# Kernel tuning notes

Measured on AMD Instinct MI355X. Metric: run time of the kernel, lower is better.

## Reference

```python
import jax, jax.numpy as jnp
import numpy as np

SEQ, EMBED, H, QLR, KVLR, RD, VD = 4096, 2048, 16, 512, 512, 64, 128
KD = VD + RD  # full key/query head dim (content + rope)


def _make_rotary_pe(seq_len, dim):
    inv_freq = 1.0 / jnp.power(10000.0, jnp.arange(0, dim, 2) / dim)
    t = jnp.arange(seq_len)
    freqs = jnp.outer(t, inv_freq)  # (seq, dim//2)
    return jnp.sin(freqs), jnp.cos(freqs)


def _apply_rope(x, sin, cos):
    # x: (seq, ..., dim); sin/cos: (seq, dim//2)
    d = x.shape[-1] // 2
    x1, x2 = x[..., :d], x[..., d:]
    sin2 = jnp.concatenate([sin, sin], axis=-1)
    cos2 = jnp.concatenate([cos, cos], axis=-1)
    ne = x.ndim - 2
    sin2 = sin2.reshape(sin2.shape[0], *[1] * ne, sin2.shape[1])
    cos2 = cos2.reshape(cos2.shape[0], *[1] * ne, cos2.shape[1])
    rot = jnp.concatenate([-x2, x1], axis=-1)
    return x * cos2 + rot * sin2


def setup_inputs() -> dict:
    key = jax.random.key(0)
    ks = jax.random.split(key, 8)

    def w(k, out_dim, in_dim):
        return jax.random.normal(k, (out_dim, in_dim), dtype=jnp.float32) * (1.0 / np.sqrt(in_dim))

    x = jax.random.normal(ks[0], (SEQ, EMBED), dtype=jnp.float32)
    mask = jnp.tril(jnp.ones((SEQ, SEQ), dtype=bool))  # causal
    return {
        "x": x,
        "mask": mask,
        "w_q_down": w(ks[1], QLR, EMBED),
        "w_q_up": w(ks[2], H * VD, QLR),
        "w_q_rope": w(ks[3], H * RD, QLR),
        "w_kv_down": w(ks[4], KVLR, EMBED),
        "w_kv_up": w(ks[5], H * 2 * VD, KVLR),
        "w_k_rope": w(ks[6], RD, EMBED),
        "w_out": w(ks[7], EMBED, H * VD),
    }


def reference(x, mask, w_q_down, w_q_up, w_q_rope, w_kv_down, w_kv_up, w_k_rope, w_out):
    seq = x.shape[0]
    # query path through low-rank bottleneck
    c_q = x @ w_q_down.T                                   # (S, QLR)
    q_content = (c_q @ w_q_up.T).reshape(seq, H, VD)       # (S, H, VD)
    q_rope = (c_q @ w_q_rope.T).reshape(seq, H, RD)        # (S, H, RD)
    # kv path through shared low-rank bottleneck
    c_kv = x @ w_kv_down.T                                 # (S, KVLR)
    kv = c_kv @ w_kv_up.T                                  # (S, H*2*VD)
    k_content_flat, v_flat = jnp.split(kv, 2, axis=-1)
    k_content = k_content_flat.reshape(seq, H, VD)
    v = v_flat.reshape(seq, H, VD)
    # shared rope key (one per token, broadcast to heads)
    k_rope_shared = (x @ w_k_rope.T)[:, None, :]           # (S, 1, RD)
    sin, cos = _make_rotary_pe(seq, RD)
    q_rope_rot = _apply_rope(q_rope, sin, cos)             # (S, H, RD)
    k_rope_rot = jnp.tile(_apply_rope(k_rope_shared, sin, cos), (1, H, 1))
    q_final = jnp.concatenate([q_content, q_rope_rot], axis=-1)  # (S, H, KD)
    k_final = jnp.concatenate([k_content, k_rope_rot], axis=-1)  # (S, H, KD)
    # values zero-padded to key dim
    v_padded = jnp.concatenate(
        [v, jnp.zeros((seq, H, RD), dtype=v.dtype)], axis=-1)    # (S, H, KD)
    # scaled dot-product attention per head
    scale = 1.0 / jnp.sqrt(jnp.asarray(KD, dtype=x.dtype))
    scores = jnp.einsum("shd,thd->hst", q_final, k_final) * scale  # (H, S, S)
    scores = jnp.where(mask[None, :, :], scores, jnp.asarray(-1e9, dtype=scores.dtype))
    probs = jax.nn.softmax(scores, axis=-1)
    attn = jnp.einsum("hst,thd->shd", probs, v_padded)             # (S, H, KD)
    attn = attn[..., :VD].reshape(seq, H * VD)                     # drop zero-pad dims
    return attn @ w_out.T                                          # (S, EMBED)
```

## Files before the change

### kernel.cpp

```cpp
#include <hip/hip_runtime.h>


#define SEQ   4096
#define EMBED 2048
#define NHEAD 16
#define QLR   512
#define KVLR  512
#define RD    64
#define VD    128
#define KDIM  192

typedef __attribute__((ext_vector_type(8)))  _Float16 half8;
typedef __attribute__((ext_vector_type(4)))  _Float16 half4;
typedef __attribute__((ext_vector_type(4)))  float    f32x4;
typedef __attribute__((ext_vector_type(16))) float    f32x16;
typedef __attribute__((ext_vector_type(2)))  unsigned int uint2v;
typedef __attribute__((ext_vector_type(4)))  unsigned int uint4v;

__device__ __forceinline__ void gload16(void* lds, const void* g) {
    __builtin_amdgcn_global_load_lds(
        (const __attribute__((address_space(1))) void*)g,
        (__attribute__((address_space(3))) void*)lds, 16, 0, 0);
}

__device__ __forceinline__ unsigned int pkh(float a, float b) {
    auto h = __builtin_amdgcn_cvt_pkrtz(a, b);
    return __builtin_bit_cast(unsigned int, h);
}

__global__ __launch_bounds__(256) void cvt_plain(const float* __restrict__ s,
                                                 _Float16* __restrict__ d, int n8) {
    const int i = blockIdx.x * 256 + threadIdx.x;
    if (i >= n8) return;
    const float4 a = reinterpret_cast<const float4*>(s)[i * 2];
    const float4 b = reinterpret_cast<const float4*>(s)[i * 2 + 1];
    half8 r;
    r[0] = (_Float16)a.x; r[1] = (_Float16)a.y; r[2] = (_Float16)a.z; r[3] = (_Float16)a.w;
    r[4] = (_Float16)b.x; r[5] = (_Float16)b.y; r[6] = (_Float16)b.z; r[7] = (_Float16)b.w;
    reinterpret_cast<half8*>(d)[i] = r;
}

__global__ __launch_bounds__(256) void cvt_down(const float* __restrict__ wqd,
                                                const float* __restrict__ wkvd,
                                                const float* __restrict__ wkr,
                                                _Float16* __restrict__ dst) {
    const int i = blockIdx.x * 256 + threadIdx.x;
    if (i >= 1152 * 2048 / 8) return;
    const int e = i * 8, row = e >> 11, col = e & 2047;
    const float* src = row < 512  ? wqd  + (size_t)row * 2048 + col
                     : row < 1024 ? wkvd + (size_t)(row - 512) * 2048 + col
                     : row < 1088 ? wkr  + (size_t)(row - 1024) * 2048 + col
                                  : nullptr;
    half8 r = {};
    if (src) {
        const float4 a = reinterpret_cast<const float4*>(src)[0];
        const float4 b = reinterpret_cast<const float4*>(src)[1];
        r[0] = (_Float16)a.x; r[1] = (_Float16)a.y; r[2] = (_Float16)a.z; r[3] = (_Float16)a.w;
        r[4] = (_Float16)b.x; r[5] = (_Float16)b.y; r[6] = (_Float16)b.z; r[7] = (_Float16)b.w;
    }
    reinterpret_cast<half8*>(dst)[i] = r;
}

__global__ __launch_bounds__(256) void cvt_qup(const float* __restrict__ wqu,
                                               const float* __restrict__ wqr,
                                               _Float16* __restrict__ dst) {
    const int i = blockIdx.x * 256 + threadIdx.x;
    if (i >= 3072 * 512 / 8) return;
    const int e = i * 8, row = e >> 9, col = e & 511;
    const float* src = row < 2048 ? wqu + (size_t)row * 512 + col
                                  : wqr + (size_t)(row - 2048) * 512 + col;
    const float4 a = reinterpret_cast<const float4*>(src)[0];
    const float4 b = reinterpret_cast<const float4*>(src)[1];
    half8 r;
    r[0] = (_Float16)a.x; r[1] = (_Float16)a.y; r[2] = (_Float16)a.z; r[3] = (_Float16)a.w;
    r[4] = (_Float16)b.x; r[5] = (_Float16)b.y; r[6] = (_Float16)b.z; r[7] = (_Float16)b.w;
    reinterpret_cast<half8*>(dst)[i] = r;
}

template <int EPI>
__global__ __launch_bounds__(256) void gemm_f16(const _Float16* __restrict__ A,
                                                const _Float16* __restrict__ B,
                                                _Float16* __restrict__ o0,
                                                _Float16* __restrict__ o1,
                                                _Float16* __restrict__ o2,
                                                float* __restrict__ of,
                                                int M, int N, int K)
{
    __shared__ _Float16 sA[128 * 64];
    __shared__ _Float16 sB[128 * 64];

    const int tid  = threadIdx.x;
    const int wid  = tid >> 6;
    const int lane = tid & 63;
    const int lr   = lane & 15;
    const int lg   = lane >> 4;
    const int row0 = blockIdx.y * 128;
    const int col0 = blockIdx.x * 128;
    const int war  = (wid >> 1) * 64;
    const int wac  = (wid & 1) * 64;

    const int sr = lane >> 3;
    const int sk = (lane & 7) * 8;
    const _Float16* Ab = A + (size_t)(row0 + wid * 8 + sr) * K + sk;
    const _Float16* Bb = B + (size_t)(col0 + wid * 8 + sr) * K + sk;

    f32x4 acc[4][4] = {};

    for (int k0 = 0; k0 < K; k0 += 64) {
#pragma unroll
        for (int i = 0; i < 4; ++i) {
            const int c = i * 4 + wid;
            gload16((char*)sA + c * 1024, Ab + (size_t)i * 32 * K + k0);
            gload16((char*)sB + c * 1024, Bb + (size_t)i * 32 * K + k0);
        }
        __syncthreads();

#pragma unroll
        for (int kk = 0; kk < 64; kk += 32) {
            half8 a[4], b[4];
#pragma unroll
            for (int i = 0; i < 4; ++i)
                a[i] = *reinterpret_cast<const half8*>(&sA[(war + i * 16 + lr) * 64 + kk + lg * 8]);
#pragma unroll
            for (int j = 0; j < 4; ++j)
                b[j] = *reinterpret_cast<const half8*>(&sB[(wac + j * 16 + lr) * 64 + kk + lg * 8]);
            __builtin_amdgcn_s_setprio(1);
#pragma unroll
            for (int i = 0; i < 4; ++i)
#pragma unroll
                for (int j = 0; j < 4; ++j)
                    acc[i][j] = __builtin_amdgcn_mfma_f32_16x16x32_f16(a[i], b[j], acc[i][j], 0, 0, 0);
            __builtin_amdgcn_s_setprio(0);
        }
        __syncthreads();
    }

#pragma unroll
    for (int i = 0; i < 4; ++i)
#pragma unroll
        for (int j = 0; j < 4; ++j) {
            const int grow0 = row0 + war + i * 16 + lg * 4;
            const int gcol  = col0 + wac + j * 16 + lr;
            if constexpr (EPI == 2) {
                if (gcol >= 2048) {
                    half4 pv;
#pragma unroll
                    for (int r = 0; r < 4; ++r) pv[r] = (_Float16)acc[i][j][r];
                    *reinterpret_cast<half4*>(&o1[(size_t)(gcol - 2048) * SEQ + grow0]) = pv;
                    continue;
                }
            }
#pragma unroll
            for (int r = 0; r < 4; ++r) {
                const int grow = grow0 + r;
                const float v = acc[i][j][r];
                if constexpr (EPI == 0) {
                    if (gcol < 512)       o0[(size_t)grow * 512 + gcol] = (_Float16)v;
                    else if (gcol < 1024) o1[(size_t)grow * 512 + gcol - 512] = (_Float16)v;
                    else if (gcol < 1088) o2[(size_t)grow * 64 + gcol - 1024] = (_Float16)v;
                } else if constexpr (EPI == 1) {
                    if (gcol < 2048)
                        o0[(size_t)grow * (NHEAD * KDIM) + (gcol >> 7) * KDIM + (gcol & 127)] = (_Float16)v;
                    else {
                        const int c = gcol - 2048;
                        o0[(size_t)grow * (NHEAD * KDIM) + (c >> 6) * KDIM + VD + (c & 63)] = (_Float16)v;
                    }
                } else if constexpr (EPI == 2) {
                    o0[((size_t)(gcol >> 7) * SEQ + grow) * KDIM + (gcol & 127)] = (_Float16)v;
                } else {
                    of[(size_t)grow * N + gcol] = v;
                }
            }
        }
}

__global__ __launch_bounds__(256) void rope_kernel(_Float16* __restrict__ qf,
                                                   _Float16* __restrict__ kf,
                                                   const _Float16* __restrict__ ktmp)
{
    __shared__ float s_sin[32], s_cos[32];
    const int s   = blockIdx.x;
    const int tid = threadIdx.x;
    if (tid < 32) {
        const double inv = exp(-(double)tid * (log(10000.0) / 32.0));
        const double ang = (double)s * inv;
        s_sin[tid] = (float)sin(ang);
        s_cos[tid] = (float)cos(ang);
    }
    __syncthreads();

    for (int p = tid; p < NHEAD * 32; p += 256) {
        const int h = p >> 5, i = p & 31;
        const size_t base = (size_t)s * (NHEAD * KDIM) + h * KDIM + VD;
        const float x1 = (float)qf[base + i];
        const float x2 = (float)qf[base + 32 + i];
        const float cs = s_cos[i], sn = s_sin[i];
        qf[base + i]      = (_Float16)(x1 * cs - x2 * sn);
        qf[base + 32 + i] = (_Float16)(x2 * cs + x1 * sn);
    }
    if (tid < 32) {
        const int i = tid;
        const float x1 = (float)ktmp[(size_t)s * RD + i];
        const float x2 = (float)ktmp[(size_t)s * RD + 32 + i];
        const float cs = s_cos[i], sn = s_sin[i];
        const _Float16 r1 = (_Float16)(x1 * cs - x2 * sn);
        const _Float16 r2 = (_Float16)(x2 * cs + x1 * sn);
#pragma unroll
        for (int h = 0; h < NHEAD; ++h) {
            const size_t base = ((size_t)h * SEQ + s) * KDIM + VD;
            kf[base + i]      = r1;
            kf[base + 32 + i] = r2;
        }
    }
}

__global__ __launch_bounds__(256, 2) void fattn(const _Float16* __restrict__ qf,
                                                const _Float16* __restrict__ kf,
                                                const _Float16* __restrict__ vT,
                                                _Float16* __restrict__ attn)
{
    __shared__ _Float16 sK[2][64 * 192];
    __shared__ _Float16 sV[128 * 64];

    const int idx = blockIdx.x;
    const int h   = idx & 15;
    const int j   = idx >> 4;
    const int qt  = (j < 16) ? (31 - 2 * j) : (2 * (j - 16));
    const int q0  = qt * 128;

    const int tid  = threadIdx.x;
    const int wid  = tid >> 6;
    const int lane = tid & 63;
    const int l31  = lane & 31;
    const int h5   = lane >> 5;
    const int x7   = l31 & 7;
    const int qg   = q0 + wid * 32 + l31;
    const int q0w  = q0 + wid * 32;

    const float scale = 0.0721687836487032f;

    const _Float16* ksrc[6];
    int klds[6];
#pragma unroll
    for (int i = 0; i < 6; ++i) {
        const int c   = wid * 6 + i;
        const int gi  = c * 64 + lane;
        const int row = gi / 24;
        const int g   = gi % 24;
        ksrc[i] = kf + ((size_t)h * SEQ + row) * KDIM + ((g ^ (row & 7)) << 3);
        klds[i] = c * 1024;
    }
    const _Float16* vsrc[4];
    int vlds[4];
#pragma unroll
    for (int i = 0; i < 4; ++i) {
        const int c = wid * 4 + i;
        const int d = c * 8 + (lane >> 3);
        vsrc[i] = vT + ((size_t)h * VD + d) * SEQ + (((lane & 7) ^ (lane >> 3)) << 3);
        vlds[i] = c * 1024;
    }

    half8 qfr[12];
    {
        const _Float16* qb_ = qf + (size_t)qg * (NHEAD * KDIM) + h * KDIM + h5 * 8;
#pragma unroll
        for (int ks = 0; ks < 12; ++ks)
            qfr[ks] = *reinterpret_cast<const half8*>(qb_ + ks * 16);
    }

    f32x16 o0 = {}, o1 = {}, o2 = {}, o3 = {};
    float m_ = -1e30f, l_ = 0.0f;

    const int nt = 2 * qt + 2;

    {
#pragma unroll
        for (int i = 0; i < 6; ++i) gload16((char*)sK[0] + klds[i], ksrc[i]);
#pragma unroll
        for (int i = 0; i < 4; ++i) gload16((char*)sV + vlds[i], vsrc[i]);
    }
    __syncthreads();

    int cur = 0;
    for (int t = 0; t < nt; ++t) {
        const int j0 = t * 64;

        if (t + 1 < nt) {
            const size_t joff = (size_t)(j0 + 64) * KDIM;
#pragma unroll
            for (int i = 0; i < 6; ++i)
                gload16((char*)sK[cur ^ 1] + klds[i], ksrc[i] + joff);
        }

        f32x16 s0 = {}, s1 = {};
        {
            const char* kb = (const char*)sK[cur];
            __builtin_amdgcn_s_setprio(1);
#pragma unroll
            for (int ks = 0; ks < 12; ++ks) {
                const int go = ((ks * 2 + h5) ^ x7) << 4;
                const half8 ka = *reinterpret_cast<const half8*>(kb + l31 * 384 + go);
                const half8 kc = *reinterpret_cast<const half8*>(kb + (32 + l31) * 384 + go);
                s0 = __builtin_amdgcn_mfma_f32_32x32x16_f16(ka, qfr[ks], s0, 0, 0, 0);
                s1 = __builtin_amdgcn_mfma_f32_32x32x16_f16(kc, qfr[ks], s1, 0, 0, 0);
            }
            __builtin_amdgcn_s_setprio(0);
        }

#pragma unroll
        for (int m = 0; m < 16; ++m) { s0[m] *= scale; s1[m] *= scale; }
        if (j0 + 63 > q0w) {
#pragma unroll
            for (int m = 0; m < 16; ++m) {
                const int kv = j0 + (m & 3) + 8 * (m >> 2) + 4 * h5;
                if (kv > qg)      s0[m] = -3.0e38f;
                if (kv + 32 > qg) s1[m] = -3.0e38f;
            }
        }

        float mx = s0[0];
#pragma unroll
        for (int m = 1; m < 16; ++m) mx = fmaxf(mx, s0[m]);
#pragma unroll
        for (int m = 0; m < 16; ++m) mx = fmaxf(mx, s1[m]);
        mx = fmaxf(mx, __shfl_xor(mx, 32, 64));

        if (!__all(mx - m_ <= 8.0f)) {
            const float mn = fmaxf(m_, mx);
            const float alpha = __expf(m_ - mn);
            m_ = mn;
            l_ *= alpha;
#pragma unroll
            for (int m = 0; m < 16; ++m) {
                o0[m] *= alpha; o1[m] *= alpha; o2[m] *= alpha; o3[m] *= alpha;
            }
        }
        float rs = 0.0f;
#pragma unroll
        for (int m = 0; m < 16; ++m) { const float p = __expf(s0[m] - m_); s0[m] = p; rs += p; }
#pragma unroll
        for (int m = 0; m < 16; ++m) { const float p = __expf(s1[m] - m_); s1[m] = p; rs += p; }
        rs += __shfl_xor(rs, 32, 64);
        l_ += rs;

        half8 pb0, pb1, pb2, pb3;
        {
            unsigned int x, x2, y, y2;
            x  = pkh(s0[0], s0[1]);  x2 = pkh(s0[2], s0[3]);
            y  = pkh(s0[4], s0[5]);  y2 = pkh(s0[6], s0[7]);
            uint2v r1 = __builtin_amdgcn_permlane32_swap(x, y, false, false);
            uint2v r2 = __builtin_amdgcn_permlane32_swap(x2, y2, false, false);
            { uint4v u = { r1[0], r2[0], r1[1], r2[1] }; pb0 = __builtin_bit_cast(half8, u); }
            x  = pkh(s0[8], s0[9]);  x2 = pkh(s0[10], s0[11]);
            y  = pkh(s0[12], s0[13]); y2 = pkh(s0[14], s0[15]);
            r1 = __builtin_amdgcn_permlane32_swap(x, y, false, false);
            r2 = __builtin_amdgcn_permlane32_swap(x2, y2, false, false);
            { uint4v u = { r1[0], r2[0], r1[1], r2[1] }; pb1 = __builtin_bit_cast(half8, u); }
            x  = pkh(s1[0], s1[1]);  x2 = pkh(s1[2], s1[3]);
            y  = pkh(s1[4], s1[5]);  y2 = pkh(s1[6], s1[7]);
            r1 = __builtin_amdgcn_permlane32_swap(x, y, false, false);
            r2 = __builtin_amdgcn_permlane32_swap(x2, y2, false, false);
            { uint4v u = { r1[0], r2[0], r1[1], r2[1] }; pb2 = __builtin_bit_cast(half8, u); }
            x  = pkh(s1[8], s1[9]);  x2 = pkh(s1[10], s1[11]);
            y  = pkh(s1[12], s1[13]); y2 = pkh(s1[14], s1[15]);
            r1 = __builtin_amdgcn_permlane32_swap(x, y, false, false);
            r2 = __builtin_amdgcn_permlane32_swap(x2, y2, false, false);
            { uint4v u = { r1[0], r2[0], r1[1], r2[1] }; pb3 = __builtin_bit_cast(half8, u); }
        }

        __syncthreads();

        {
            const char* vbse = (const char*)sV;
            __builtin_amdgcn_s_setprio(1);
#pragma unroll
            for (int ks = 0; ks < 4; ++ks) {
                const int go = ((ks * 2 + h5) ^ x7) << 4;
                const half8 pbk = ks == 0 ? pb0 : ks == 1 ? pb1 : ks == 2 ? pb2 : pb3;
                const half8 v0 = *reinterpret_cast<const half8*>(vbse + (l31)      * 128 + go);
                const half8 v1 = *reinterpret_cast<const half8*>(vbse + (32 + l31) * 128 + go);
                const half8 v2 = *reinterpret_cast<const half8*>(vbse + (64 + l31) * 128 + go);
                const half8 v3 = *reinterpret_cast<const half8*>(vbse + (96 + l31) * 128 + go);
                o0 = __builtin_amdgcn_mfma_f32_32x32x16_f16(v0, pbk, o0, 0, 0, 0);
                o1 = __builtin_amdgcn_mfma_f32_32x32x16_f16(v1, pbk, o1, 0, 0, 0);
                o2 = __builtin_amdgcn_mfma_f32_32x32x16_f16(v2, pbk, o2, 0, 0, 0);
                o3 = __builtin_amdgcn_mfma_f32_32x32x16_f16(v3, pbk, o3, 0, 0, 0);
            }
            __builtin_amdgcn_s_setprio(0);
        }

        __syncthreads();

        if (t + 1 < nt) {
            const int jn = j0 + 64;
#pragma unroll
            for (int i = 0; i < 4; ++i)
                gload16((char*)sV + vlds[i], vsrc[i] + jn);
        }
        cur ^= 1;
    }

    const float invl = 1.0f / l_;
    _Float16* ob = attn + (size_t)qg * (NHEAD * VD) + h * VD + 4 * h5;
#pragma unroll
    for (int g = 0; g < 4; ++g) {
#pragma unroll
        for (int pp = 0; pp < 2; ++pp) {
            const int m = g * 4 + pp * 2;
            const int dof = pp * 2 + 8 * g;
            *reinterpret_cast<unsigned int*>(ob + dof) =
                pkh(o0[m] * invl, o0[m + 1] * invl);
            *reinterpret_cast<unsigned int*>(ob + 32 + dof) =
                pkh(o1[m] * invl, o1[m + 1] * invl);
            *reinterpret_cast<unsigned int*>(ob + 64 + dof) =
                pkh(o2[m] * invl, o2[m + 1] * invl);
            *reinterpret_cast<unsigned int*>(ob + 96 + dof) =
                pkh(o3[m] * invl, o3[m + 1] * invl);
        }
    }
}

extern "C" void kernel_launch(void* const* d_in, const int* in_sizes, int n_in,
                              void* d_out, int out_size, void* d_ws, size_t ws_size,
                              hipStream_t stream)
{
    (void)in_sizes; (void)n_in; (void)out_size; (void)ws_size;
    const float* x    = (const float*)d_in[0];
    const float* wqd  = (const float*)d_in[2];
    const float* wqu  = (const float*)d_in[3];
    const float* wqr  = (const float*)d_in[4];
    const float* wkvd = (const float*)d_in[5];
    const float* wkvu = (const float*)d_in[6];
    const float* wkr  = (const float*)d_in[7];
    const float* wout = (const float*)d_in[8];
    float* out = (float*)d_out;

    char* ws = (char*)d_ws;
    _Float16* x_h    = (_Float16*)ws; ws += (size_t)SEQ * EMBED * 2;
    _Float16* wdownh = (_Float16*)ws; ws += (size_t)1152 * EMBED * 2;
    _Float16* wquph  = (_Float16*)ws; ws += (size_t)3072 * QLR * 2;
    _Float16* wkvuh  = (_Float16*)ws; ws += (size_t)4096 * KVLR * 2;
    _Float16* c_q    = (_Float16*)ws; ws += (size_t)SEQ * QLR * 2;
    _Float16* c_kv   = (_Float16*)ws; ws += (size_t)SEQ * KVLR * 2;
    _Float16* ktmp   = (_Float16*)ws; ws += (size_t)SEQ * RD * 2;
    _Float16* qfin   = (_Float16*)ws; ws += (size_t)SEQ * NHEAD * KDIM * 2;
    _Float16* kfin   = (_Float16*)ws; ws += (size_t)SEQ * NHEAD * KDIM * 2;
    _Float16* vT     = (_Float16*)ws; ws += (size_t)NHEAD * VD * SEQ * 2;
    _Float16* attn   = x_h;
    _Float16* wouth  = c_q;

    dim3 blk(256);

    cvt_plain<<<dim3(4096), blk, 0, stream>>>(x, x_h, SEQ * EMBED / 8);
    cvt_down <<<dim3(1152), blk, 0, stream>>>(wqd, wkvd, wkr, wdownh);
    cvt_qup  <<<dim3(768),  blk, 0, stream>>>(wqu, wqr, wquph);
    cvt_plain<<<dim3(1024), blk, 0, stream>>>(wkvu, wkvuh, 4096 * KVLR / 8);

    gemm_f16<0><<<dim3(9, 32), blk, 0, stream>>>(
        x_h, wdownh, c_q, c_kv, ktmp, nullptr, SEQ, 1152, EMBED);
    gemm_f16<1><<<dim3(24, 32), blk, 0, stream>>>(
        c_q, wquph, qfin, nullptr, nullptr, nullptr, SEQ, 3072, QLR);
    gemm_f16<2><<<dim3(32, 32), blk, 0, stream>>>(
        c_kv, wkvuh, kfin, vT, nullptr, nullptr, SEQ, 4096, KVLR);

    cvt_plain<<<dim3(2048), blk, 0, stream>>>(wout, wouth, EMBED * EMBED / 8);

    rope_kernel<<<dim3(SEQ), blk, 0, stream>>>(qfin, kfin, ktmp);
    fattn<<<dim3(512), blk, 0, stream>>>(qfin, kfin, vT, attn);
    gemm_f16<3><<<dim3(16, 32), blk, 0, stream>>>(
        attn, wouth, nullptr, nullptr, nullptr, out, SEQ, EMBED, NHEAD * VD);
}
```

Measured before the change: 335.7 us.

## Merge conversion kernels and use fine-grained waitcnt barriers in attention loop

The four fp32-to-fp16 conversion launches are merged into one kernel that dispatches on block index, removing three launches. In the flash-attention loop, the full __syncthreads calls are replaced with explicit vmcnt/lgkmcnt waits plus raw s_barrier. Each wait covers only the loads needed at that point, so the next K tile's prefetch can stay in flight. The hand-counted vmcnt values are fragile and rely on how many global_load_lds ops are outstanding; a miscount would introduce a race.

```diff
diff --git a/kernel.cpp b/kernel.cpp
--- a/kernel.cpp
+++ b/kernel.cpp
@@ -28,53 +28,58 @@
     return __builtin_bit_cast(unsigned int, h);
 }
 
+__device__ __forceinline__ half8 cvt8(const float* p) {
+    const float4 a = *reinterpret_cast<const float4*>(p);
+    const float4 b = *reinterpret_cast<const float4*>(p + 4);
+    half8 r;
+    r[0] = (_Float16)a.x; r[1] = (_Float16)a.y; r[2] = (_Float16)a.z; r[3] = (_Float16)a.w;
+    r[4] = (_Float16)b.x; r[5] = (_Float16)b.y; r[6] = (_Float16)b.z; r[7] = (_Float16)b.w;
+    return r;
+}
+
+__global__ __launch_bounds__(256) void cvt_all(const float* __restrict__ x,
+                                               const float* __restrict__ wqd,
+                                               const float* __restrict__ wkvd,
+                                               const float* __restrict__ wkr,
+                                               const float* __restrict__ wqu,
+                                               const float* __restrict__ wqr,
+                                               const float* __restrict__ wkvu,
+                                               _Float16* __restrict__ x_h,
+                                               _Float16* __restrict__ wdownh,
+                                               _Float16* __restrict__ wquph,
+                                               _Float16* __restrict__ wkvuh)
+{
+    const int b = blockIdx.x;
+    if (b < 4096) {
+        const int i = b * 256 + threadIdx.x;
+        reinterpret_cast<half8*>(x_h)[i] = cvt8(x + i * 8);
+    } else if (b < 5248) {
+        const int i = (b - 4096) * 256 + threadIdx.x;
+        const int e = i * 8, row = e >> 11, col = e & 2047;
+        const float* src = row < 512  ? wqd  + (size_t)row * 2048 + col
+                         : row < 1024 ? wkvd + (size_t)(row - 512) * 2048 + col
+                         : row < 1088 ? wkr  + (size_t)(row - 1024) * 2048 + col
+                                      : nullptr;
+        half8 r = {};
+        if (src) r = cvt8(src);
+        reinterpret_cast<half8*>(wdownh)[i] = r;
+    } else if (b < 6016) {
+        const int i = (b - 5248) * 256 + threadIdx.x;
+        const int e = i * 8, row = e >> 9, col = e & 511;
+        const float* src = row < 2048 ? wqu + (size_t)row * 512 + col
+                                      : wqr + (size_t)(row - 2048) * 512 + col;
+        reinterpret_cast<half8*>(wquph)[i] = cvt8(src);
+    } else {
+        const int i = (b - 6016) * 256 + threadIdx.x;
+        reinterpret_cast<half8*>(wkvuh)[i] = cvt8(wkvu + i * 8);
+    }
+}
+
 __global__ __launch_bounds__(256) void cvt_plain(const float* __restrict__ s,
                                                  _Float16* __restrict__ d, int n8) {
     const int i = blockIdx.x * 256 + threadIdx.x;
     if (i >= n8) return;
-    const float4 a = reinterpret_cast<const float4*>(s)[i * 2];
-    const float4 b = reinterpret_cast<const float4*>(s)[i * 2 + 1];
-    half8 r;
-    r[0] = (_Float16)a.x; r[1] = (_Float16)a.y; r[2] = (_Float16)a.z; r[3] = (_Float16)a.w;
-    r[4] = (_Float16)b.x; r[5] = (_Float16)b.y; r[6] = (_Float16)b.z; r[7] = (_Float16)b.w;
-    reinterpret_cast<half8*>(d)[i] = r;
-}
-
-__global__ __launch_bounds__(256) void cvt_down(const float* __restrict__ wqd,
-                                                const float* __restrict__ wkvd,
-                                                const float* __restrict__ wkr,
-                                                _Float16* __restrict__ dst) {
-    const int i = blockIdx.x * 256 + threadIdx.x;
-    if (i >= 1152 * 2048 / 8) return;
-    const int e = i * 8, row = e >> 11, col = e & 2047;
-    const float* src = row < 512  ? wqd  + (size_t)row * 2048 + col
-                     : row < 1024 ? wkvd + (size_t)(row - 512) * 2048 + col
-                     : row < 1088 ? wkr  + (size_t)(row - 1024) * 2048 + col
-                                  : nullptr;
-    half8 r = {};
-    if (src) {
-        const float4 a = reinterpret_cast<const float4*>(src)[0];
-        const float4 b = reinterpret_cast<const float4*>(src)[1];
-        r[0] = (_Float16)a.x; r[1] = (_Float16)a.y; r[2] = (_Float16)a.z; r[3] = (_Float16)a.w;
-        r[4] = (_Float16)b.x; r[5] = (_Float16)b.y; r[6] = (_Float16)b.z; r[7] = (_Float16)b.w;
-    }
-    reinterpret_cast<half8*>(dst)[i] = r;
-}
-
-__global__ __launch_bounds__(256) void cvt_qup(const float* __restrict__ wqu,
-                                               const float* __restrict__ wqr,
-                                               _Float16* __restrict__ dst) {
-    const int i = blockIdx.x * 256 + threadIdx.x;
-    if (i >= 3072 * 512 / 8) return;
-    const int e = i * 8, row = e >> 9, col = e & 511;
-    const float* src = row < 2048 ? wqu + (size_t)row * 512 + col
-                                  : wqr + (size_t)(row - 2048) * 512 + col;
-    const float4 a = reinterpret_cast<const float4*>(src)[0];
-    const float4 b = reinterpret_cast<const float4*>(src)[1];
-    half8 r;
-    r[0] = (_Float16)a.x; r[1] = (_Float16)a.y; r[2] = (_Float16)a.z; r[3] = (_Float16)a.w;
-    r[4] = (_Float16)b.x; r[5] = (_Float16)b.y; r[6] = (_Float16)b.z; r[7] = (_Float16)b.w;
-    reinterpret_cast<half8*>(dst)[i] = r;
+    reinterpret_cast<half8*>(d)[i] = cvt8(s + i * 8);
 }
 
 template <int EPI>
@@ -273,19 +278,18 @@
 
     const int nt = 2 * qt + 2;
 
-    {
-#pragma unroll
-        for (int i = 0; i < 6; ++i) gload16((char*)sK[0] + klds[i], ksrc[i]);
-#pragma unroll
-        for (int i = 0; i < 4; ++i) gload16((char*)sV + vlds[i], vsrc[i]);
-    }
+#pragma unroll
+    for (int i = 0; i < 6; ++i) gload16((char*)sK[0] + klds[i], ksrc[i]);
+#pragma unroll
+    for (int i = 0; i < 4; ++i) gload16((char*)sV + vlds[i], vsrc[i]);
     __syncthreads();
 
     int cur = 0;
     for (int t = 0; t < nt; ++t) {
         const int j0 = t * 64;
-
-        if (t + 1 < nt) {
+        const bool more = (t + 1 < nt);
+
+        if (more) {
             const size_t joff = (size_t)(j0 + 64) * KDIM;
 #pragma unroll
             for (int i = 0; i < 6; ++i)
@@ -368,7 +372,10 @@
             { uint4v u = { r1[0], r2[0], r1[1], r2[1] }; pb3 = __builtin_bit_cast(half8, u); }
         }
 
-        __syncthreads();
+        if (more) asm volatile("s_waitcnt vmcnt(6)" ::: "memory");
+        else      asm volatile("s_waitcnt vmcnt(0)" ::: "memory");
+        __builtin_amdgcn_sched_barrier(0);
+        __builtin_amdgcn_s_barrier();
 
         {
             const char* vbse = (const char*)sV;
@@ -389,13 +396,18 @@
             __builtin_amdgcn_s_setprio(0);
         }
 
-        __syncthreads();
-
-        if (t + 1 < nt) {
+        asm volatile("s_waitcnt lgkmcnt(0)" ::: "memory");
+        __builtin_amdgcn_sched_barrier(0);
+        __builtin_amdgcn_s_barrier();
+
+        if (more) {
             const int jn = j0 + 64;
 #pragma unroll
             for (int i = 0; i < 4; ++i)
                 gload16((char*)sV + vlds[i], vsrc[i] + jn);
+            asm volatile("s_waitcnt vmcnt(4)" ::: "memory");
+            __builtin_amdgcn_sched_barrier(0);
+            __builtin_amdgcn_s_barrier();
         }
         cur ^= 1;
     }
@@ -451,10 +463,8 @@
 
     dim3 blk(256);
 
-    cvt_plain<<<dim3(4096), blk, 0, stream>>>(x, x_h, SEQ * EMBED / 8);
-    cvt_down <<<dim3(1152), blk, 0, stream>>>(wqd, wkvd, wkr, wdownh);
-    cvt_qup  <<<dim3(768),  blk, 0, stream>>>(wqu, wqr, wquph);
-    cvt_plain<<<dim3(1024), blk, 0, stream>>>(wkvu, wkvuh, 4096 * KVLR / 8);
+    cvt_all<<<dim3(7040), blk, 0, stream>>>(x, wqd, wkvd, wkr, wqu, wqr, wkvu,
+                                            x_h, wdownh, wquph, wkvuh);
 
     gemm_f16<0><<<dim3(9, 32), blk, 0, stream>>>(
         x_h, wdownh, c_q, c_kv, ktmp, nullptr, SEQ, 1152, EMBED);
```

Result: no change. 332.6 us (-0.9%).
